# Kernel optimization log

Measured on AMD Instinct MI355X. Metric: run time of the kernel, lower is better.

Reference implementation:

```python
import jax, jax.numpy as jnp
import numpy as np

B, S, DIM = 1, 2048, 2048
H = 16
Q_LORA, KV_LORA = 1536, 512
D_NOPE, D_ROPE, D_V = 128, 64, 128
D_QK = D_NOPE + D_ROPE  # 192
EPS = 1e-6


def rms_norm(x, w, eps=EPS):
    var = jnp.mean(jnp.square(x), axis=-1, keepdims=True)
    return x * jax.lax.rsqrt(var + eps) * w


def apply_rope(x, cos, sin):
    # x: [B,S,H,D] with interleaved complex pairs; cos/sin: [S,D//2]
    x1, x2 = x[..., 0::2], x[..., 1::2]
    c = cos[None, :, None, :]
    s = sin[None, :, None, :]
    o1 = x1 * c - x2 * s
    o2 = x1 * s + x2 * c
    return jnp.stack([o1, o2], axis=-1).reshape(x.shape)


def setup_inputs() -> dict:
    key = jax.random.key(0)
    ks = jax.random.split(key, 8)
    x = jax.random.normal(ks[0], (B, S, DIM), dtype=jnp.float32)
    # rotary tables (standard complex exponentials)
    inv_freq = 1.0 / (10000.0 ** (np.arange(0, D_ROPE, 2, dtype=np.float32) / D_ROPE))
    t = np.arange(S, dtype=np.float32)
    freqs = np.outer(t, inv_freq)  # [S, D_ROPE//2]
    freqs_cos = jnp.asarray(np.cos(freqs))
    freqs_sin = jnp.asarray(np.sin(freqs))
    sd = lambda fan_in: 1.0 / np.sqrt(fan_in)
    wq_a = jax.random.normal(ks[1], (Q_LORA, DIM), dtype=jnp.float32) * sd(DIM)
    q_a_ln_w = jnp.ones((Q_LORA,), dtype=jnp.float32)
    wq_b = jax.random.normal(ks[2], (H * D_QK, Q_LORA), dtype=jnp.float32) * sd(Q_LORA)
    wkv_a = jax.random.normal(ks[3], (KV_LORA + D_ROPE, DIM), dtype=jnp.float32) * sd(DIM)
    kv_a_ln_w = jnp.ones((KV_LORA,), dtype=jnp.float32)
    wkv_b = jax.random.normal(ks[4], (H * (D_NOPE + D_V), KV_LORA), dtype=jnp.float32) * sd(KV_LORA)
    wo = jax.random.normal(ks[5], (DIM, H * D_V), dtype=jnp.float32) * sd(H * D_V)
    return {"x": x, "freqs_cos": freqs_cos, "freqs_sin": freqs_sin,
            "wq_a": wq_a, "q_a_ln_w": q_a_ln_w, "wq_b": wq_b,
            "wkv_a": wkv_a, "kv_a_ln_w": kv_a_ln_w, "wkv_b": wkv_b, "wo": wo}


def reference(x, freqs_cos, freqs_sin, wq_a, q_a_ln_w, wq_b, wkv_a, kv_a_ln_w, wkv_b, wo):
    softmax_scale = D_QK ** -0.5
    # Query: low-rank down-proj -> RMSNorm -> up-proj
    q = rms_norm(x @ wq_a.T, q_a_ln_w) @ wq_b.T            # [B,S,H*D_QK]
    q = q.reshape(B, S, H, D_QK)
    q_nope, q_pe = q[..., :D_NOPE], q[..., D_NOPE:]
    q_pe = apply_rope(q_pe, freqs_cos, freqs_sin)
    # KV: shared low-rank latent + decoupled rope key (MQA-style, 1 head)
    kv = x @ wkv_a.T                                        # [B,S,KV_LORA+D_ROPE]
    kv_c = rms_norm(kv[..., :KV_LORA], kv_a_ln_w)           # [B,S,KV_LORA]
    k_pe = apply_rope(kv[..., None, KV_LORA:], freqs_cos, freqs_sin)  # [B,S,1,D_ROPE]
    kvb = (kv_c @ wkv_b.T).reshape(B, S, H, D_NOPE + D_V)
    k_nope, v = kvb[..., :D_NOPE], kvb[..., D_NOPE:]
    # Attention scores: nope part + shared rope part
    scores = (jnp.einsum('bqhd,bkhd->bhqk', q_nope, k_nope)
              + jnp.einsum('bqhd,bkd->bhqk', q_pe, k_pe[:, :, 0, :])) * softmax_scale
    causal = jnp.tril(jnp.ones((S, S), dtype=bool))
    scores = jnp.where(causal[None, None], scores, -jnp.inf)
    p = jax.nn.softmax(scores, axis=-1)
    out = jnp.einsum('bhqk,bkhd->bqhd', p, v).reshape(B, S, H * D_V)
    return out @ wo.T
```

## Files before the change

kernel.cpp:

```cpp
#include <hip/hip_runtime.h>
#include <cstdint>
#include <cstddef>

typedef __bf16 bf16;
typedef bf16 bf16x8 __attribute__((ext_vector_type(8)));
typedef bf16 bf16x4 __attribute__((ext_vector_type(4)));
typedef float f32x4 __attribute__((ext_vector_type(4)));

typedef __attribute__((address_space(1))) void as1_void;
typedef __attribute__((address_space(3))) void as3_void;

#define INF __builtin_inff()

__global__ __launch_bounds__(256) void z100_cast_all(
    const float* __restrict__ x, const float* __restrict__ wq_a,
    const float* __restrict__ wkv_a, const float* __restrict__ wq_b,
    const float* __restrict__ wkv_b, const float* __restrict__ wo,
    bf16* __restrict__ x_bf, bf16* __restrict__ wab_bf,
    bf16* __restrict__ wqb_bf, bf16* __restrict__ wkvb_bf,
    bf16* __restrict__ wo_bf) {
    int i = blockIdx.x * 256 + threadIdx.x;
    const float* s;
    bf16* d;
    float mul = 1.f;
    if (i < 1048576)      { s = x + (size_t)i * 4;                     d = x_bf + (size_t)i * 4; }
    else if (i < 1835008) { int o = i - 1048576; s = wq_a  + (size_t)o * 4; d = wab_bf + (size_t)o * 4; }
    else if (i < 2129920) { int o = i - 1835008; s = wkv_a + (size_t)o * 4; d = wab_bf + 1536ull * 2048 + (size_t)o * 4; }
    else if (i < 3309568) { int o = i - 2129920; s = wq_b  + (size_t)o * 4; d = wqb_bf + (size_t)o * 4;
                            mul = 0.072168783649f; }
    else if (i < 3833856) { int o = i - 3309568; s = wkv_b + (size_t)o * 4; d = wkvb_bf + (size_t)o * 4; }
    else if (i < 4882432) { int o = i - 3833856; s = wo    + (size_t)o * 4; d = wo_bf + (size_t)o * 4; }
    else {                  int o = i - 4882432; bf16x4 z = {};
                            *(bf16x4*)(wab_bf + 2112ull * 2048 + (size_t)o * 4) = z; return; }
    float4 v = *(const float4*)s;
    bf16x4 ovec = { (bf16)(v.x * mul), (bf16)(v.y * mul), (bf16)(v.z * mul), (bf16)(v.w * mul) };
    *(bf16x4*)d = ovec;
}

__global__ __launch_bounds__(256) void z100_rmsnorm_bf(
    const bf16* __restrict__ x, int ldx, const float* __restrict__ w,
    bf16* __restrict__ y, int N, float invN) {
    const int row = blockIdx.x;
    const bf16* xr = x + (size_t)row * ldx;
    float ss = 0.f;
    for (int i = threadIdx.x * 8; i < N; i += 2048) {
        bf16x8 v = *(const bf16x8*)(xr + i);
        #pragma unroll
        for (int j = 0; j < 8; ++j) { float f = (float)v[j]; ss += f * f; }
    }
    #pragma unroll
    for (int d = 1; d < 64; d <<= 1) ss += __shfl_xor(ss, d);
    __shared__ float red[4];
    if ((threadIdx.x & 63) == 0) red[threadIdx.x >> 6] = ss;
    __syncthreads();
    float tot = red[0] + red[1] + red[2] + red[3];
    float rs = rsqrtf(tot * invN + 1e-6f);
    bf16* yr = y + (size_t)row * N;
    for (int i = threadIdx.x * 8; i < N; i += 2048) {
        bf16x8 v = *(const bf16x8*)(xr + i);
        float4 w0 = *(const float4*)(w + i);
        float4 w1 = *(const float4*)(w + i + 4);
        bf16x8 o;
        o[0] = (bf16)((float)v[0] * rs * w0.x); o[1] = (bf16)((float)v[1] * rs * w0.y);
        o[2] = (bf16)((float)v[2] * rs * w0.z); o[3] = (bf16)((float)v[3] * rs * w0.w);
        o[4] = (bf16)((float)v[4] * rs * w1.x); o[5] = (bf16)((float)v[5] * rs * w1.y);
        o[6] = (bf16)((float)v[6] * rs * w1.z); o[7] = (bf16)((float)v[7] * rs * w1.w);
        *(bf16x8*)(yr + i) = o;
    }
}

template <typename OutT>
__device__ __forceinline__ void gemm8_body(
    const bf16* __restrict__ A, const bf16* __restrict__ B,
    OutT* __restrict__ C, int N, int K, int ldc, int mblk, int nblk,
    bf16* AsB, bf16* BsB) {
    const int tid = threadIdx.x;
    const int lane = tid & 63, wave = tid >> 6;
    const int l15 = lane & 15, l4 = lane >> 4;
    const int m0 = mblk * 128, n0 = nblk * 128;
    const int wr = (wave >> 1) * 32, wc = (wave & 1) * 64;

    f32x4 acc[2][4] = {};

    const int srow = lane >> 2;
    const int scol = (lane & 3) * 8;
    const size_t a_base = (size_t)(m0 + wave * 16 + srow) * K + scol;
    const size_t b_base = (size_t)(n0 + wave * 16 + srow) * K + scol;

    auto stg = [&](int buf, int k0) {
        __builtin_amdgcn_global_load_lds((as1_void*)(void*)(A + a_base + k0),
                                         (as3_void*)(AsB + buf * 4096 + wave * 512), 16, 0, 0);
        __builtin_amdgcn_global_load_lds((as1_void*)(void*)(B + b_base + k0),
                                         (as3_void*)(BsB + buf * 4096 + wave * 512), 16, 0, 0);
    };

    const int nt = K >> 5;
    stg(0, 0);
    stg(1, 32);
    asm volatile("s_waitcnt vmcnt(2)" ::: "memory");
    __builtin_amdgcn_s_barrier();

    int cb = 0, sb = 2;
    for (int t = 0; t < nt; ++t) {
        if (t + 2 < nt) stg(sb, (t + 2) * 32);
        const bf16* Ab = AsB + cb * 4096;
        const bf16* Bb = BsB + cb * 4096;
        bf16x8 fa[2], fb[4];
        #pragma unroll
        for (int i = 0; i < 2; ++i)
            fa[i] = *(const bf16x8*)(Ab + (wr + 16 * i + l15) * 32 + 8 * l4);
        #pragma unroll
        for (int j = 0; j < 4; ++j)
            fb[j] = *(const bf16x8*)(Bb + (wc + 16 * j + l15) * 32 + 8 * l4);
        #pragma unroll
        for (int i = 0; i < 2; ++i)
            #pragma unroll
            for (int j = 0; j < 4; ++j)
                acc[i][j] = __builtin_amdgcn_mfma_f32_16x16x32_bf16(fa[i], fb[j], acc[i][j], 0, 0, 0);
        if (t + 2 < nt) { asm volatile("s_waitcnt vmcnt(2)" ::: "memory"); }
        else            { asm volatile("s_waitcnt vmcnt(0)" ::: "memory"); }
        __builtin_amdgcn_s_barrier();
        cb = (cb == 2) ? 0 : cb + 1;
        sb = (sb == 2) ? 0 : sb + 1;
    }

    #pragma unroll
    for (int i = 0; i < 2; ++i) {
        int row0 = m0 + wr + 16 * i + 4 * l4;
        #pragma unroll
        for (int j = 0; j < 4; ++j) {
            int col = n0 + wc + 16 * j + l15;
            if (col < N) {
                #pragma unroll
                for (int jj = 0; jj < 4; ++jj)
                    C[(size_t)(row0 + jj) * ldc + col] = (OutT)acc[i][j][jj];
            }
        }
    }
}

__global__ __launch_bounds__(512) void z100_gemm8(
    const bf16* __restrict__ A, const bf16* __restrict__ B,
    float* __restrict__ C, int N, int K, int ldc) {
    __shared__ alignas(16) bf16 As[3 * 128 * 32];
    __shared__ alignas(16) bf16 Bs[3 * 128 * 32];
    gemm8_body<float>(A, B, C, N, K, ldc, blockIdx.y, blockIdx.x, As, Bs);
}

__global__ __launch_bounds__(512) void z100_gemm8_bf(
    const bf16* __restrict__ A, const bf16* __restrict__ B,
    bf16* __restrict__ C, int N, int K, int ldc) {
    __shared__ alignas(16) bf16 As[3 * 128 * 32];
    __shared__ alignas(16) bf16 Bs[3 * 128 * 32];
    gemm8_body<bf16>(A, B, C, N, K, ldc, blockIdx.y, blockIdx.x, As, Bs);
}

__global__ __launch_bounds__(512) void z100_gemm_qkv(
    const bf16* __restrict__ qan, const bf16* __restrict__ wqb, bf16* __restrict__ qf,
    const bf16* __restrict__ kvc, const bf16* __restrict__ wkvb, bf16* __restrict__ kvbf) {
    __shared__ alignas(16) bf16 As[3 * 128 * 32];
    __shared__ alignas(16) bf16 Bs[3 * 128 * 32];
    const int bid = blockIdx.x;
    if (bid < 384) gemm8_body<bf16>(qan, wqb, qf, 3072, 1536, 3072, bid / 24, bid % 24, As, Bs);
    else { int b = bid - 384; gemm8_body<bf16>(kvc, wkvb, kvbf, 4096, 512, 4096, b / 32, b % 32, As, Bs); }
}

__global__ void z100_pe_prep(const bf16* __restrict__ q_f, const bf16* __restrict__ qa,
                             const float* __restrict__ fc, const float* __restrict__ fs,
                             bf16* __restrict__ qpe, bf16* __restrict__ kpe) {
    const int QTOT = 2048 * 16 * 32;
    int u = blockIdx.x * 256 + threadIdx.x;
    if (u < QTOT) {
        int i = u & 31;
        int h = (u >> 5) & 15;
        int s = u >> 9;
        float c = fc[s * 32 + i], sn = fs[s * 32 + i];
        float x1 = (float)q_f[(size_t)s * 3072 + h * 192 + 128 + 2 * i];
        float x2 = (float)q_f[(size_t)s * 3072 + h * 192 + 128 + 2 * i + 1];
        qpe[(size_t)s * 1024 + h * 64 + 2 * i]     = (bf16)(x1 * c - x2 * sn);
        qpe[(size_t)s * 1024 + h * 64 + 2 * i + 1] = (bf16)(x1 * sn + x2 * c);
    } else {
        int v = u - QTOT;
        int i = v & 31;
        int s = v >> 5;
        float c = fc[s * 32 + i], sn = fs[s * 32 + i];
        float x1 = (float)qa[(size_t)s * 2112 + 2048 + 2 * i];
        float x2 = (float)qa[(size_t)s * 2112 + 2048 + 2 * i + 1];
        kpe[(size_t)s * 64 + 2 * i]     = (bf16)(x1 * c - x2 * sn);
        kpe[(size_t)s * 64 + 2 * i + 1] = (bf16)(x1 * sn + x2 * c);
    }
}

__global__ __launch_bounds__(256) void z100_v_trans(const bf16* __restrict__ kvb,
                                                    bf16* __restrict__ vt) {
    const int st = blockIdx.x, h = blockIdx.y;
    const int s0 = st * 64;
    __shared__ alignas(16) bf16 tile[64 * 132];
    const int tid = threadIdx.x;
    #pragma unroll
    for (int i = 0; i < 4; ++i) {
        int slot = i * 256 + tid;
        int r = slot >> 4, c8 = slot & 15;
        bf16x8 v = *(const bf16x8*)(kvb + (size_t)(s0 + r) * 4096 + h * 256 + 128 + c8 * 8);
        *(bf16x8*)(tile + r * 132 + c8 * 8) = v;
    }
    __syncthreads();
    #pragma unroll
    for (int i = 0; i < 4; ++i) {
        int slot = i * 256 + tid;
        int d = slot >> 3, ch = slot & 7;
        bf16x8 o;
        #pragma unroll
        for (int j = 0; j < 8; ++j) o[j] = tile[(ch * 8 + j) * 132 + d];
        *(bf16x8*)(vt + ((size_t)h * 128 + d) * 2048 + s0 + ch * 8) = o;
    }
}

__global__ __launch_bounds__(512) void z100_attn(
    const bf16* __restrict__ q_f, const bf16* __restrict__ qpe,
    const bf16* __restrict__ kvb, const bf16* __restrict__ kpe,
    const bf16* __restrict__ v_t, bf16* __restrict__ opart, float* __restrict__ ml) {
    const int bid = blockIdx.x;
    const int wk = (bid & 7) * 80 + (bid >> 3);
    const int h = wk / 40;
    const int s0w = wk - h * 40;
    int qt = 0, rem = s0w;
    while (rem >= (qt >> 2) + 1) { rem -= (qt >> 2) + 1; ++qt; }
    const int chk = rem;
    const int q0 = qt * 128;
    const int kstart = chk * 512;
    const int kend = min(q0 + 128, kstart + 512);
    const int slot = h * 40 + s0w;

    const int tid = threadIdx.x;
    const int lane = tid & 63, wave = tid >> 6;
    const int l15 = lane & 15, l4 = lane >> 4;

    __shared__ alignas(16) bf16 Ks[2][64 * 192];
    __shared__ alignas(16) bf16 Vs[2][128 * 64];

    const bf16* Vh = v_t + (size_t)h * 128 * 2048;

    const int wrow_max = q0 + wave * 16 + 15;
    const int diag_k0 = q0 + (wave >> 2) * 64;

    bf16x8 qf[6];
    {
        const int qrow = q0 + wave * 16 + l15;
        const bf16* qn = q_f + (size_t)qrow * 3072 + h * 192 + 8 * l4;
        #pragma unroll
        for (int c = 0; c < 4; ++c) qf[c] = *(const bf16x8*)(qn + 32 * c);
        const bf16* qp = qpe + (size_t)qrow * 1024 + h * 64 + 8 * l4;
        qf[4] = *(const bf16x8*)(qp);
        qf[5] = *(const bf16x8*)(qp + 32);
    }

    const bf16* kp0[3];
    int kstep[3];
    #pragma unroll
    for (int i = 0; i < 3; ++i) {
        int off = (wave * 3 + i) * 1024 + lane * 16;
        int r = off / 384;
        int ch = (off % 384) >> 4;
        int ksrc = (r & 0x23) | ((r & 0x0C) << 1) | ((r & 0x10) >> 2);
        int chx = ch ^ (r & 7);
        if (chx < 16) { kp0[i] = kvb + (size_t)ksrc * 4096 + h * 256 + chx * 8; kstep[i] = 4096; }
        else          { kp0[i] = kpe + (size_t)ksrc * 64 + (chx - 16) * 8;      kstep[i] = 64; }
    }
    int voff[2];
    #pragma unroll
    for (int i = 0; i < 2; ++i) {
        int off = (wave * 2 + i) * 1024 + lane * 16;
        int d = off >> 7;
        int ch = (off >> 4) & 7;
        voff[i] = d * 2048 + (ch ^ (d & 7)) * 8;
    }

    auto stage = [&](int buf, int k0) {
        #pragma unroll
        for (int i = 0; i < 3; ++i)
            __builtin_amdgcn_global_load_lds(
                (as1_void*)(void*)(kp0[i] + (size_t)k0 * kstep[i]),
                (as3_void*)((char*)&Ks[buf][0] + (wave * 3 + i) * 1024), 16, 0, 0);
        #pragma unroll
        for (int i = 0; i < 2; ++i)
            __builtin_amdgcn_global_load_lds(
                (as1_void*)(void*)(Vh + k0 + voff[i]),
                (as3_void*)((char*)&Vs[buf][0] + (wave * 2 + i) * 1024), 16, 0, 0);
    };

    f32x4 oacc[8] = {};
    float m_r = -INF, l_r = 0.f;
    const int nt = (kend - kstart) >> 6;

    stage(0, kstart);
    __syncthreads();
    int cur = 0;
    for (int t = 0; t < nt; ++t) {
        const int k0 = kstart + t * 64;
        if (t + 1 < nt) stage(cur ^ 1, k0 + 64);

        if (k0 <= wrow_max) {
            const char* KsC = (const char*)&Ks[cur][0];
            const char* VsC = (const char*)&Vs[cur][0];

            f32x4 sc[4];
            __builtin_amdgcn_s_setprio(1);
            #pragma unroll
            for (int kt = 0; kt < 4; ++kt) {
                f32x4 a = { 0.f, 0.f, 0.f, 0.f };
                int r = 16 * kt + l15;
                #pragma unroll
                for (int c = 0; c < 6; ++c) {
                    int byteo = (r * 384 + c * 64 + l4 * 16) ^ ((r & 7) << 4);
                    bf16x8 kf = *(const bf16x8*)(KsC + byteo);
                    a = __builtin_amdgcn_mfma_f32_16x16x32_bf16(kf, qf[c], a, 0, 0, 0);
                }
                sc[kt] = a;
            }
            __builtin_amdgcn_s_setprio(0);

            if (k0 == diag_k0) {
                int qrow = (wave & 3) * 16 + l15;
                #pragma unroll
                for (int kt = 0; kt < 4; ++kt)
                    #pragma unroll
                    for (int r = 0; r < 4; ++r) {
                        int kl = ((kt >> 1) << 5) | (l4 << 3) | ((kt & 1) << 2) | r;
                        if (kl > qrow) sc[kt][r] = -INF;
                    }
            }

            float mx = -INF;
            #pragma unroll
            for (int kt = 0; kt < 4; ++kt)
                #pragma unroll
                for (int r = 0; r < 4; ++r) mx = fmaxf(mx, sc[kt][r]);
            mx = fmaxf(mx, __shfl_xor(mx, 16));
            mx = fmaxf(mx, __shfl_xor(mx, 32));
            float mnew = fmaxf(m_r, mx);
            float corr = __expf(m_r - mnew);
            float rs = 0.f;
            #pragma unroll
            for (int kt = 0; kt < 4; ++kt)
                #pragma unroll
                for (int r = 0; r < 4; ++r) {
                    float pv = __expf(sc[kt][r] - mnew);
                    sc[kt][r] = pv;
                    rs += pv;
                }
            rs += __shfl_xor(rs, 16);
            rs += __shfl_xor(rs, 32);
            l_r = l_r * corr + rs;
            m_r = mnew;

            float c_r[4];
            #pragma unroll
            for (int r = 0; r < 4; ++r) c_r[r] = __shfl(corr, 20 * l4 + r);
            #pragma unroll
            for (int dt = 0; dt < 8; ++dt)
                #pragma unroll
                for (int r = 0; r < 4; ++r) oacc[dt][r] *= c_r[r];

            bf16x8 pf[2];
            #pragma unroll
            for (int c2 = 0; c2 < 2; ++c2)
                #pragma unroll
                for (int i = 0; i < 8; ++i)
                    pf[c2][i] = (bf16)sc[2 * c2 + (i >> 2)][i & 3];

            __builtin_amdgcn_s_setprio(1);
            #pragma unroll
            for (int dt = 0; dt < 8; ++dt) {
                #pragma unroll
                for (int c2 = 0; c2 < 2; ++c2) {
                    int d = 16 * dt + l15;
                    int byteo = (d * 128 + c2 * 64 + l4 * 16) ^ ((d & 7) << 4);
                    bf16x8 vf = *(const bf16x8*)(VsC + byteo);
                    oacc[dt] = __builtin_amdgcn_mfma_f32_16x16x32_bf16(pf[c2], vf, oacc[dt], 0, 0, 0);
                }
            }
            __builtin_amdgcn_s_setprio(0);
        }

        __syncthreads();
        cur ^= 1;
    }

    const int qr_base = wave * 16;
    if (lane < 16) {
        ml[(size_t)slot * 256 + qr_base + lane] = m_r;
        ml[(size_t)slot * 256 + 128 + qr_base + lane] = l_r;
    }
    bf16* ob = opart + (size_t)slot * 16384;
    #pragma unroll
    for (int dt = 0; dt < 8; ++dt) {
        int d = 16 * dt + l15;
        #pragma unroll
        for (int r = 0; r < 4; ++r) {
            int qr = qr_base + 4 * l4 + r;
            ob[qr * 128 + d] = (bf16)oacc[dt][r];
        }
    }
}

__global__ __launch_bounds__(512) void z100_attn_combine(
    const bf16* __restrict__ opart, const float* __restrict__ ml, bf16* __restrict__ ao) {
    const int qt = blockIdx.x, h = blockIdx.y;
    const int t = threadIdx.x;
    const int np = (qt >> 2) + 1;
    int base = 0;
    for (int j = 0; j < qt; ++j) base += (j >> 2) + 1;
    const int slot0 = h * 40 + base;
    #pragma unroll 1
    for (int it = 0; it < 4; ++it) {
        const int c = it * 512 + t;
        const int qr = c >> 4;
        const int dc = (c & 15) * 8;
        float m[4], l[4], w[4];
        float M = -INF;
        #pragma unroll
        for (int i = 0; i < 4; ++i)
            if (i < np) {
                m[i] = ml[(size_t)(slot0 + i) * 256 + qr];
                l[i] = ml[(size_t)(slot0 + i) * 256 + 128 + qr];
                M = fmaxf(M, m[i]);
            }
        float L = 0.f;
        #pragma unroll
        for (int i = 0; i < 4; ++i)
            if (i < np) {
                w[i] = __expf(m[i] - M);
                L += w[i] * l[i];
            }
        float invL = 1.f / L;
        float acc[8] = {};
        #pragma unroll
        for (int i = 0; i < 4; ++i)
            if (i < np) {
                bf16x8 a = *(const bf16x8*)(opart + (size_t)(slot0 + i) * 16384 + (size_t)c * 8);
                #pragma unroll
                for (int j = 0; j < 8; ++j) acc[j] += w[i] * (float)a[j];
            }
        bf16x8 o;
        #pragma unroll
        for (int j = 0; j < 8; ++j) o[j] = (bf16)(acc[j] * invL);
        *(bf16x8*)(ao + (size_t)(qt * 128 + qr) * 2048 + h * 128 + dc) = o;
    }
}

extern "C" void kernel_launch(void* const* d_in, const int* in_sizes, int n_in,
                              void* d_out, int out_size, void* d_ws, size_t ws_size,
                              hipStream_t stream) {
    (void)in_sizes; (void)n_in; (void)out_size; (void)ws_size;
    const float* x     = (const float*)d_in[0];
    const float* fc    = (const float*)d_in[1];
    const float* fs    = (const float*)d_in[2];
    const float* wq_a  = (const float*)d_in[3];
    const float* q_ln  = (const float*)d_in[4];
    const float* wq_b  = (const float*)d_in[5];
    const float* wkv_a = (const float*)d_in[6];
    const float* kv_ln = (const float*)d_in[7];
    const float* wkv_b = (const float*)d_in[8];
    const float* wo    = (const float*)d_in[9];
    float* out = (float*)d_out;

    char* p = (char*)d_ws;
    auto alloc = [&](size_t bytes) {
        char* r = p;
        p += (bytes + 255) & ~(size_t)255;
        return r;
    };
    char* phase1  = p;
    bf16* x_bf    = (bf16*)alloc(2048ull * 2048 * 2);
    bf16* wab_bf  = (bf16*)alloc(2176ull * 2048 * 2);
    bf16* qa_bf   = (bf16*)alloc(2048ull * 2112 * 2);
    bf16* qan_bf  = (bf16*)alloc(2048ull * 1536 * 2);
    bf16* wqb_bf  = (bf16*)alloc(3072ull * 1536 * 2);
    bf16* wkvb_bf = (bf16*)alloc(4096ull * 512 * 2);
    bf16* wo_bf   = (bf16*)alloc(2048ull * 2048 * 2);
    bf16* q_f     = (bf16*)alloc(2048ull * 3072 * 2);
    bf16* kvc_bf  = (bf16*)alloc(2048ull * 512 * 2);
    bf16* kvb_f   = (bf16*)alloc(2048ull * 4096 * 2);
    bf16* qpe     = (bf16*)alloc(2048ull * 16 * 64 * 2);
    bf16* kpe     = (bf16*)alloc(2048ull * 64 * 2);
    bf16* v_t     = (bf16*)alloc(16ull * 128 * 2048 * 2);
    bf16* ao_bf   = (bf16*)alloc(2048ull * 2048 * 2);
    bf16* opart   = (bf16*)phase1;
    float* mlbuf  = (float*)(phase1 + 640ull * 16384 * 2);

    z100_cast_all<<<19200, 256, 0, stream>>>(x, wq_a, wkv_a, wq_b, wkv_b, wo,
                                             x_bf, wab_bf, wqb_bf, wkvb_bf, wo_bf);

    z100_gemm8_bf<<<dim3(17, 16), 512, 0, stream>>>(x_bf, wab_bf, qa_bf, 2112, 2048, 2112);
    z100_rmsnorm_bf<<<2048, 256, 0, stream>>>(qa_bf, 2112, q_ln, qan_bf, 1536, 1.f / 1536.f);
    z100_rmsnorm_bf<<<2048, 256, 0, stream>>>(qa_bf + 1536, 2112, kv_ln, kvc_bf, 512, 1.f / 512.f);

    z100_gemm_qkv<<<dim3(896), 512, 0, stream>>>(qan_bf, wqb_bf, q_f, kvc_bf, wkvb_bf, kvb_f);

    z100_pe_prep<<<4352, 256, 0, stream>>>(q_f, qa_bf, fc, fs, qpe, kpe);
    z100_v_trans<<<dim3(32, 16), 256, 0, stream>>>(kvb_f, v_t);

    z100_attn<<<dim3(640), 512, 0, stream>>>(q_f, qpe, kvb_f, kpe, v_t, opart, mlbuf);
    z100_attn_combine<<<dim3(16, 16), 512, 0, stream>>>(opart, mlbuf, ao_bf);

    z100_gemm8<<<dim3(16, 16), 512, 0, stream>>>(ao_bf, wo_bf, out, 2048, 2048, 2048);
}
```

Before: 224.3 us.

## Merge small kernels, add XCD-aware block remap, and lazy softmax rescale

Merges the two RMSNorm launches into one kernel and the rope-prep and V-transpose kernels into one prep kernel, which cuts launch count and per-launch overhead. Adds an XCD-striding block index remap to the GEMM kernels so that neighbouring tiles land on the same chiplet and share L2. In attention, the online-softmax max update and accumulator rescale are skipped unless the new block max exceeds the running max by more than a threshold, which saves exp and multiply work. The lazy rescale lets unnormalised exponentials grow up to e^8, which stays safe in fp32 but changes rounding slightly.

```diff
diff --git a/kernel.cpp b/kernel.cpp
--- a/kernel.cpp
+++ b/kernel.cpp
@@ -37,11 +37,17 @@
     *(bf16x4*)d = ovec;
 }
 
-__global__ __launch_bounds__(256) void z100_rmsnorm_bf(
-    const bf16* __restrict__ x, int ldx, const float* __restrict__ w,
-    bf16* __restrict__ y, int N, float invN) {
-    const int row = blockIdx.x;
-    const bf16* xr = x + (size_t)row * ldx;
+__global__ __launch_bounds__(256) void z100_rmsnorm2(
+    const bf16* __restrict__ qa, const float* __restrict__ q_ln,
+    const float* __restrict__ kv_ln,
+    bf16* __restrict__ qan, bf16* __restrict__ kvc) {
+    const int bid = blockIdx.x;
+    const bf16* xr;
+    const float* w;
+    bf16* yr;
+    int N; float invN;
+    if (bid < 2048) { xr = qa + (size_t)bid * 2112;        w = q_ln;  yr = qan + (size_t)bid * 1536; N = 1536; invN = 1.f / 1536.f; }
+    else { int r = bid - 2048; xr = qa + (size_t)r * 2112 + 1536; w = kv_ln; yr = kvc + (size_t)r * 512;  N = 512;  invN = 1.f / 512.f; }
     float ss = 0.f;
     for (int i = threadIdx.x * 8; i < N; i += 2048) {
         bf16x8 v = *(const bf16x8*)(xr + i);
@@ -55,7 +61,6 @@
     __syncthreads();
     float tot = red[0] + red[1] + red[2] + red[3];
     float rs = rsqrtf(tot * invN + 1e-6f);
-    bf16* yr = y + (size_t)row * N;
     for (int i = threadIdx.x * 8; i < N; i += 2048) {
         bf16x8 v = *(const bf16x8*)(xr + i);
         float4 w0 = *(const float4*)(w + i);
@@ -139,12 +144,22 @@
     }
 }
 
+__device__ __forceinline__ void xcd_decode(int gx, int& mblk, int& nblk) {
+    int total = gx * gridDim.y;
+    int bid = blockIdx.y * gx + blockIdx.x;
+    int w = (bid & 7) * (total >> 3) + (bid >> 3);
+    nblk = w % gx;
+    mblk = w / gx;
+}
+
 __global__ __launch_bounds__(512) void z100_gemm8(
     const bf16* __restrict__ A, const bf16* __restrict__ B,
     float* __restrict__ C, int N, int K, int ldc) {
     __shared__ alignas(16) bf16 As[3 * 128 * 32];
     __shared__ alignas(16) bf16 Bs[3 * 128 * 32];
-    gemm8_body<float>(A, B, C, N, K, ldc, blockIdx.y, blockIdx.x, As, Bs);
+    int mblk, nblk;
+    xcd_decode(gridDim.x, mblk, nblk);
+    gemm8_body<float>(A, B, C, N, K, ldc, mblk, nblk, As, Bs);
 }
 
 __global__ __launch_bounds__(512) void z100_gemm8_bf(
@@ -152,7 +167,9 @@
     bf16* __restrict__ C, int N, int K, int ldc) {
     __shared__ alignas(16) bf16 As[3 * 128 * 32];
     __shared__ alignas(16) bf16 Bs[3 * 128 * 32];
-    gemm8_body<bf16>(A, B, C, N, K, ldc, blockIdx.y, blockIdx.x, As, Bs);
+    int mblk, nblk;
+    xcd_decode(gridDim.x, mblk, nblk);
+    gemm8_body<bf16>(A, B, C, N, K, ldc, mblk, nblk, As, Bs);
 }
 
 __global__ __launch_bounds__(512) void z100_gemm_qkv(
@@ -161,15 +178,43 @@
     __shared__ alignas(16) bf16 As[3 * 128 * 32];
     __shared__ alignas(16) bf16 Bs[3 * 128 * 32];
     const int bid = blockIdx.x;
-    if (bid < 384) gemm8_body<bf16>(qan, wqb, qf, 3072, 1536, 3072, bid / 24, bid % 24, As, Bs);
-    else { int b = bid - 384; gemm8_body<bf16>(kvc, wkvb, kvbf, 4096, 512, 4096, b / 32, b % 32, As, Bs); }
-}
-
-__global__ void z100_pe_prep(const bf16* __restrict__ q_f, const bf16* __restrict__ qa,
-                             const float* __restrict__ fc, const float* __restrict__ fs,
-                             bf16* __restrict__ qpe, bf16* __restrict__ kpe) {
+    const int w = (bid & 7) * 112 + (bid >> 3);
+    if (w < 384) gemm8_body<bf16>(qan, wqb, qf, 3072, 1536, 3072, w / 24, w % 24, As, Bs);
+    else { int b = w - 384; gemm8_body<bf16>(kvc, wkvb, kvbf, 4096, 512, 4096, b / 32, b % 32, As, Bs); }
+}
+
+__global__ __launch_bounds__(256) void z100_prep(
+    const bf16* __restrict__ kvb, const bf16* __restrict__ q_f,
+    const bf16* __restrict__ qa,
+    const float* __restrict__ fc, const float* __restrict__ fs,
+    bf16* __restrict__ vt, bf16* __restrict__ qpe, bf16* __restrict__ kpe) {
+    const int bid = blockIdx.x;
+    const int tid = threadIdx.x;
+    if (bid < 512) {
+        const int st = bid & 31, h = bid >> 5;
+        const int s0 = st * 64;
+        __shared__ alignas(16) bf16 tile[64 * 132];
+        #pragma unroll
+        for (int i = 0; i < 4; ++i) {
+            int slot = i * 256 + tid;
+            int r = slot >> 4, c8 = slot & 15;
+            bf16x8 v = *(const bf16x8*)(kvb + (size_t)(s0 + r) * 4096 + h * 256 + 128 + c8 * 8);
+            *(bf16x8*)(tile + r * 132 + c8 * 8) = v;
+        }
+        __syncthreads();
+        #pragma unroll
+        for (int i = 0; i < 4; ++i) {
+            int slot = i * 256 + tid;
+            int d = slot >> 3, ch = slot & 7;
+            bf16x8 o;
+            #pragma unroll
+            for (int j = 0; j < 8; ++j) o[j] = tile[(ch * 8 + j) * 132 + d];
+            *(bf16x8*)(vt + ((size_t)h * 128 + d) * 2048 + s0 + ch * 8) = o;
+        }
+        return;
+    }
     const int QTOT = 2048 * 16 * 32;
-    int u = blockIdx.x * 256 + threadIdx.x;
+    int u = (bid - 512) * 256 + tid;
     if (u < QTOT) {
         int i = u & 31;
         int h = (u >> 5) & 15;
@@ -191,31 +236,6 @@
     }
 }
 
-__global__ __launch_bounds__(256) void z100_v_trans(const bf16* __restrict__ kvb,
-                                                    bf16* __restrict__ vt) {
-    const int st = blockIdx.x, h = blockIdx.y;
-    const int s0 = st * 64;
-    __shared__ alignas(16) bf16 tile[64 * 132];
-    const int tid = threadIdx.x;
-    #pragma unroll
-    for (int i = 0; i < 4; ++i) {
-        int slot = i * 256 + tid;
-        int r = slot >> 4, c8 = slot & 15;
-        bf16x8 v = *(const bf16x8*)(kvb + (size_t)(s0 + r) * 4096 + h * 256 + 128 + c8 * 8);
-        *(bf16x8*)(tile + r * 132 + c8 * 8) = v;
-    }
-    __syncthreads();
-    #pragma unroll
-    for (int i = 0; i < 4; ++i) {
-        int slot = i * 256 + tid;
-        int d = slot >> 3, ch = slot & 7;
-        bf16x8 o;
-        #pragma unroll
-        for (int j = 0; j < 8; ++j) o[j] = tile[(ch * 8 + j) * 132 + d];
-        *(bf16x8*)(vt + ((size_t)h * 128 + d) * 2048 + s0 + ch * 8) = o;
-    }
-}
-
 __global__ __launch_bounds__(512) void z100_attn(
     const bf16* __restrict__ q_f, const bf16* __restrict__ qpe,
     const bf16* __restrict__ kvb, const bf16* __restrict__ kpe,
@@ -338,29 +358,31 @@
                 for (int r = 0; r < 4; ++r) mx = fmaxf(mx, sc[kt][r]);
             mx = fmaxf(mx, __shfl_xor(mx, 16));
             mx = fmaxf(mx, __shfl_xor(mx, 32));
-            float mnew = fmaxf(m_r, mx);
-            float corr = __expf(m_r - mnew);
+            if (!__all(mx <= m_r + 8.f)) {
+                float mnew = fmaxf(m_r, mx);
+                float corr = __expf(m_r - mnew);
+                float c_r[4];
+                #pragma unroll
+                for (int r = 0; r < 4; ++r) c_r[r] = __shfl(corr, 20 * l4 + r);
+                #pragma unroll
+                for (int dt = 0; dt < 8; ++dt)
+                    #pragma unroll
+                    for (int r = 0; r < 4; ++r) oacc[dt][r] *= c_r[r];
+                l_r *= corr;
+                m_r = mnew;
+            }
             float rs = 0.f;
             #pragma unroll
             for (int kt = 0; kt < 4; ++kt)
                 #pragma unroll
                 for (int r = 0; r < 4; ++r) {
-                    float pv = __expf(sc[kt][r] - mnew);
+                    float pv = __expf(sc[kt][r] - m_r);
                     sc[kt][r] = pv;
                     rs += pv;
                 }
             rs += __shfl_xor(rs, 16);
             rs += __shfl_xor(rs, 32);
-            l_r = l_r * corr + rs;
-            m_r = mnew;
-
-            float c_r[4];
-            #pragma unroll
-            for (int r = 0; r < 4; ++r) c_r[r] = __shfl(corr, 20 * l4 + r);
-            #pragma unroll
-            for (int dt = 0; dt < 8; ++dt)
-                #pragma unroll
-                for (int r = 0; r < 4; ++r) oacc[dt][r] *= c_r[r];
+            l_r += rs;
 
             bf16x8 pf[2];
             #pragma unroll
@@ -493,13 +515,11 @@
                                              x_bf, wab_bf, wqb_bf, wkvb_bf, wo_bf);
 
     z100_gemm8_bf<<<dim3(17, 16), 512, 0, stream>>>(x_bf, wab_bf, qa_bf, 2112, 2048, 2112);
-    z100_rmsnorm_bf<<<2048, 256, 0, stream>>>(qa_bf, 2112, q_ln, qan_bf, 1536, 1.f / 1536.f);
-    z100_rmsnorm_bf<<<2048, 256, 0, stream>>>(qa_bf + 1536, 2112, kv_ln, kvc_bf, 512, 1.f / 512.f);
+    z100_rmsnorm2<<<4096, 256, 0, stream>>>(qa_bf, q_ln, kv_ln, qan_bf, kvc_bf);
 
     z100_gemm_qkv<<<dim3(896), 512, 0, stream>>>(qan_bf, wqb_bf, q_f, kvc_bf, wkvb_bf, kvb_f);
 
-    z100_pe_prep<<<4352, 256, 0, stream>>>(q_f, qa_bf, fc, fs, qpe, kpe);
-    z100_v_trans<<<dim3(32, 16), 256, 0, stream>>>(kvb_f, v_t);
+    z100_prep<<<4864, 256, 0, stream>>>(kvb_f, q_f, qa_bf, fc, fs, v_t, qpe, kpe);
 
     z100_attn<<<dim3(640), 512, 0, stream>>>(q_f, qpe, kvb_f, kpe, v_t, opart, mlbuf);
     z100_attn_combine<<<dim3(16, 16), 512, 0, stream>>>(opart, mlbuf, ao_bf);
```

Result: slower. 250.3 us (+11.6%).
